# Performance work log

Measured on AMD Instinct MI355X. Metric: run time of the kernel, lower is better.

## Reference

```python
import jax, jax.numpy as jnp
import numpy as np

H = 12
D_MODEL = 768
D_K = D_MODEL // H  # 64


def setup_inputs() -> dict:
    key = jax.random.key(0)
    ks = jax.random.split(key, 16)
    B, S, D = 4, 1024, D_MODEL
    scale = 1.0 / np.sqrt(D)
    inp = {
        "query": jax.random.normal(ks[0], (B, S, D), jnp.float32),
        "key": jax.random.normal(ks[1], (B, S, D), jnp.float32),
        "value": jax.random.normal(ks[2], (B, S, D), jnp.float32),
        "times": jax.random.normal(ks[3], (2, B, S, D), jnp.float32),
        # learned params (Linear weights stored torch-style [out, in])
        "Wq": jax.random.normal(ks[4], (D, D), jnp.float32) * scale,
        "bq": jnp.zeros((D,), jnp.float32),
        "Wk": jax.random.normal(ks[5], (D, D), jnp.float32) * scale,
        "bk": jnp.zeros((D,), jnp.float32),
        "Wv": jax.random.normal(ks[6], (D, D), jnp.float32) * scale,
        "bv": jnp.zeros((D,), jnp.float32),
        "Wt": jax.random.normal(ks[7], (D, D), jnp.float32) * scale,
        "bt": jnp.zeros((D,), jnp.float32),
        "Wo": jax.random.normal(ks[8], (D, D), jnp.float32) * scale,
        "bo": jnp.zeros((D,), jnp.float32),
    }
    return inp


def _split_heads(x, B, S):
    # [B,S,D] -> [B,H,S,D_K]
    return x.reshape(B, S, H, D_K).transpose(0, 2, 1, 3)


def reference(query, key, value, times, Wq, bq, Wk, bk, Wv, bv, Wt, bt, Wo, bo):
    B, S, D = query.shape
    inv_sqrt_dk = 1.0 / jnp.sqrt(jnp.asarray(D_K, query.dtype))
    # q/k/v projections are identical across time-loop iterations; hoist them.
    q = _split_heads(query @ Wq.T + bq, B, S)   # [B,H,S,dk]
    k = _split_heads(key @ Wk.T + bk, B, S)
    v = _split_heads(value @ Wv.T + bv, B, S)
    x = jnp.zeros_like(q)
    n_times = times.shape[0]
    for i in range(n_times):  # small fixed loop over time embeddings
        t = _split_heads(times[i] @ Wt.T + bt, B, S)
        # dual-score attention: query.time + query.key, each scaled by 1/sqrt(d_k)
        scores = (jnp.einsum('bhqd,bhkd->bhqk', q, t)
                  + jnp.einsum('bhqd,bhkd->bhqk', q, k)) * inv_sqrt_dk
        p = jax.nn.softmax(scores, axis=-1)
        x = x + jnp.einsum('bhqk,bhkd->bhqd', p, v)
    x = x.transpose(0, 2, 1, 3).reshape(B, S, H * D_K)
    return x @ Wo.T + bo
```

## Files before the change

kernel.cpp:

```cpp
#include <hip/hip_runtime.h>
#include <hip/hip_fp16.h>

typedef _Float16 v8h __attribute__((ext_vector_type(8)));
typedef _Float16 v4h __attribute__((ext_vector_type(4)));
typedef _Float16 v2h __attribute__((ext_vector_type(2)));
typedef float v4f __attribute__((ext_vector_type(4)));

#define MFMA_F16 __builtin_amdgcn_mfma_f32_16x16x32_f16
#define EXP2F __builtin_amdgcn_exp2f

__device__ static inline v2h pkrtz(float a, float b) {
  return __builtin_bit_cast(v2h, __builtin_amdgcn_cvt_pkrtz(a, b));
}

__device__ static inline void async_copy16(const void* g, void* l) {
  __builtin_amdgcn_global_load_lds(
      (const __attribute__((address_space(1))) void*)g,
      (__attribute__((address_space(3))) void*)l, 16, 0, 0);
}

struct CastArgs {
  const float* src[10];
  _Float16* dst[10];
  int start[11];
  float scale[10];
};
__global__ void cast_all(CastArgs a) {
  const int g = blockIdx.x * 256 + threadIdx.x;
  if (g >= a.start[10]) return;
  int z = 0;
  #pragma unroll
  for (int i = 1; i < 10; ++i) if (g >= a.start[i]) z = i;
  const int i0 = g - a.start[z];
  const float sc = a.scale[z];
  const float* s = a.src[z] + (size_t)i0 * 8;
  const float4 f0 = *(const float4*)s;
  const float4 f1 = *(const float4*)(s + 4);
  v8h o = {(_Float16)(f0.x * sc), (_Float16)(f0.y * sc),
           (_Float16)(f0.z * sc), (_Float16)(f0.w * sc),
           (_Float16)(f1.x * sc), (_Float16)(f1.y * sc),
           (_Float16)(f1.z * sc), (_Float16)(f1.w * sc)};
  *(v8h*)(a.dst[z] + (size_t)i0 * 8) = o;
}

struct GemmArgs {
  const _Float16* A1[4]; const _Float16* A2[4];
  const _Float16* W1[4]; const _Float16* W2[4];
  const float* b1[4];    const float* b2[4];
  void* out[4];
  float bscale[4];
  int K[4];
  int mode[4];
};

template <int MT>
__global__ __launch_bounds__(256) void gemm_mt(GemmArgs g) {
  constexpr int iA = MT / 32;
  constexpr int NMT = MT / 32;
  __shared__ _Float16 a_lds[MT * 64];
  __shared__ _Float16 w_lds[128 * 64];
  const int z = blockIdx.z;
  const int KK = g.K[z];
  const int tid = threadIdx.x;
  const int w = tid >> 6, lane = tid & 63, quad = lane >> 4, l16 = lane & 15;
  const int m0 = blockIdx.x * MT, n0 = blockIdx.y * 128;
  const int wm = (w >> 1) * (MT / 2), wn = (w & 1) * 64;

  size_t srcOff[4]; int ldsOff[4];
  #pragma unroll
  for (int i = 0; i < 4; ++i) {
    const int c = i * 256 + tid, row = c >> 3, slot = c & 7;
    srcOff[i] = (size_t)row * 768 + (size_t)((slot ^ (row & 7)) * 8);
    ldsOff[i] = (i * 256 + w * 64) * 8;
  }

  v4f acc[NMT][4] = {};

  for (int k0 = 0; k0 < KK; k0 += 64) {
    const _Float16* Asrc = (k0 < 768) ? g.A1[z] : g.A2[z];
    const _Float16* Wsrc = (k0 < 768) ? g.W1[z] : g.W2[z];
    const int kc = (k0 < 768) ? k0 : k0 - 768;
    __syncthreads();
    #pragma unroll
    for (int i = 0; i < 4; ++i) {
      if (i < iA)
        async_copy16(Asrc + (size_t)m0 * 768 + kc + srcOff[i], &a_lds[ldsOff[i]]);
      async_copy16(Wsrc + (size_t)n0 * 768 + kc + srcOff[i], &w_lds[ldsOff[i]]);
    }
    __syncthreads();

    #pragma unroll
    for (int kh = 0; kh < 2; ++kh) {
      v8h af[NMT], bf[4];
      #pragma unroll
      for (int mt = 0; mt < NMT; ++mt) {
        const int r = wm + mt * 16 + l16;
        af[mt] = *(const v8h*)&a_lds[r * 64 + (((kh * 4 + quad) ^ (r & 7)) * 8)];
      }
      #pragma unroll
      for (int nt = 0; nt < 4; ++nt) {
        const int r = wn + nt * 16 + l16;
        bf[nt] = *(const v8h*)&w_lds[r * 64 + (((kh * 4 + quad) ^ (r & 7)) * 8)];
      }
      #pragma unroll
      for (int mt = 0; mt < NMT; ++mt)
        #pragma unroll
        for (int nt = 0; nt < 4; ++nt)
          acc[mt][nt] = MFMA_F16(af[mt], bf[nt], acc[mt][nt], 0, 0, 0);
    }
  }

  const int mode = g.mode[z];
  #pragma unroll
  for (int nt = 0; nt < 4; ++nt) {
    const int col = n0 + wn + nt * 16 + l16;
    float bv = g.b1[z][col] * g.bscale[z];
    if (g.b2[z]) bv += g.b2[z][col];
    if (mode == 1) {
      _Float16* outp = (_Float16*)g.out[z];
      const int h = col >> 6, dk = col & 63;
      #pragma unroll
      for (int mt = 0; mt < NMT; ++mt) {
        const int row = m0 + wm + mt * 16 + quad * 4;
        const int b = row >> 10, s = row & 1023;
        const int sp = (s & ~31) | ((s & 12) << 1) | ((s & 16) >> 2);
        v4h pack = {(_Float16)(acc[mt][nt][0] + bv), (_Float16)(acc[mt][nt][1] + bv),
                    (_Float16)(acc[mt][nt][2] + bv), (_Float16)(acc[mt][nt][3] + bv)};
        *(v4h*)&outp[(size_t)((b * 12 + h) * 64 + dk) * 1024 + sp] = pack;
      }
    } else {
      #pragma unroll
      for (int mt = 0; mt < NMT; ++mt)
        #pragma unroll
        for (int r = 0; r < 4; ++r) {
          const int row = m0 + wm + mt * 16 + quad * 4 + r;
          const float v = acc[mt][nt][r] + bv;
          if (mode == 2) ((float*)g.out[z])[(size_t)row * 768 + col] = v;
          else ((_Float16*)g.out[z])[(size_t)row * 768 + col] = (_Float16)v;
        }
    }
  }
}

__global__ __launch_bounds__(256) void attn(
    const _Float16* __restrict__ Q,
    const _Float16* __restrict__ KT0, const _Float16* __restrict__ KT1,
    const _Float16* __restrict__ Vt,
    _Float16* __restrict__ X)
{
  __shared__ _Float16 kt0[2][64 * 64];
  __shared__ _Float16 kt1[2][64 * 64];
  __shared__ _Float16 vt[2][64 * 64];

  const int tid = threadIdx.x;
  const int w = tid >> 6, lane = tid & 63, quad = lane >> 4, l16 = lane & 15;
  const int bh = blockIdx.y, b = bh / 12, h = bh % 12;
  const int q0 = blockIdx.x * 64;
  const size_t base = (size_t)b * 1024 * 768 + h * 64;

  const _Float16* KT0b = KT0 + base;
  const _Float16* KT1b = KT1 + base;
  const _Float16* Vtb = Vt + (size_t)bh * 64 * 1024;

  size_t ktOff[2], vOff[2]; int ldsOff[2];
  #pragma unroll
  for (int i = 0; i < 2; ++i) {
    const int c = i * 256 + w * 64 + lane, row = c >> 3, slot = c & 7;
    const int logical = slot ^ (row & 7);
    ktOff[i] = (size_t)row * 768 + (size_t)(logical * 8);
    vOff[i] = (size_t)row * 1024 + (size_t)(logical * 8);
    ldsOff[i] = c * 8;
  }
  auto stage = [&](int kv0, int buf) {
    #pragma unroll
    for (int i = 0; i < 2; ++i) {
      async_copy16(KT0b + (size_t)kv0 * 768 + ktOff[i], &kt0[buf][ldsOff[i]]);
      async_copy16(KT1b + (size_t)kv0 * 768 + ktOff[i], &kt1[buf][ldsOff[i]]);
      async_copy16(Vtb + (size_t)kv0 + vOff[i], &vt[buf][ldsOff[i]]);
    }
  };

  const _Float16* Qw = Q + base + (size_t)(q0 + w * 16) * 768;
  const v8h qf0 = *(const v8h*)(Qw + (size_t)l16 * 768 + quad * 8);
  const v8h qf1 = *(const v8h*)(Qw + (size_t)l16 * 768 + 32 + quad * 8);

  const _Float16 one = (_Float16)1.f;
  const v8h ones8 = {one, one, one, one, one, one, one, one};
  v4f o[2][4] = {};
  v4f osum[2] = {};

  auto body = [&](int cc, const _Float16* k0p, const _Float16* k1p,
                  const _Float16* vp) {
    __syncthreads();
    if (cc < 15) stage((cc + 1) * 64, (cc + 1) & 1);

    v4f s[2][4];
    #pragma unroll
    for (int kvt = 0; kvt < 4; ++kvt) {
      const int r = kvt * 16 + l16, rw = r & 7;
      const v8h k00 = *(const v8h*)&k0p[r * 64 + ((quad ^ rw) * 8)];
      const v8h k01 = *(const v8h*)&k0p[r * 64 + (((4 + quad) ^ rw) * 8)];
      const v8h k10 = *(const v8h*)&k1p[r * 64 + ((quad ^ rw) * 8)];
      const v8h k11 = *(const v8h*)&k1p[r * 64 + (((4 + quad) ^ rw) * 8)];
      s[0][kvt] = MFMA_F16(k00, qf0, v4f{}, 0, 0, 0);
      s[0][kvt] = MFMA_F16(k01, qf1, s[0][kvt], 0, 0, 0);
      s[1][kvt] = MFMA_F16(k10, qf0, v4f{}, 0, 0, 0);
      s[1][kvt] = MFMA_F16(k11, qf1, s[1][kvt], 0, 0, 0);
    }

    v8h pb8[2][2];
    #pragma unroll
    for (int t = 0; t < 2; ++t)
      #pragma unroll
      for (int gg = 0; gg < 2; ++gg) {
        const v4f sa = s[t][gg * 2], sb = s[t][gg * 2 + 1];
        const v2h a0 = pkrtz(EXP2F(sa[0]), EXP2F(sa[1]));
        const v2h a1 = pkrtz(EXP2F(sa[2]), EXP2F(sa[3]));
        const v2h b0 = pkrtz(EXP2F(sb[0]), EXP2F(sb[1]));
        const v2h b1 = pkrtz(EXP2F(sb[2]), EXP2F(sb[3]));
        pb8[t][gg] = v8h{a0[0], a0[1], a1[0], a1[1], b0[0], b0[1], b1[0], b1[1]};
        osum[t] = MFMA_F16(ones8, pb8[t][gg], osum[t], 0, 0, 0);
      }

    #pragma unroll
    for (int dkt = 0; dkt < 4; ++dkt) {
      const int row = dkt * 16 + l16, rw = row & 7;
      #pragma unroll
      for (int gg = 0; gg < 2; ++gg) {
        const int slot = (gg * 4 + quad) ^ rw;
        const v8h vv = *(const v8h*)&vp[row * 64 + slot * 8];
        o[0][dkt] = MFMA_F16(vv, pb8[0][gg], o[0][dkt], 0, 0, 0);
        o[1][dkt] = MFMA_F16(vv, pb8[1][gg], o[1][dkt], 0, 0, 0);
      }
    }
  };

  stage(0, 0);
  for (int it = 0; it < 8; ++it) {
    body(it * 2, &kt0[0][0], &kt1[0][0], &vt[0][0]);
    body(it * 2 + 1, &kt0[1][0], &kt1[1][0], &vt[1][0]);
  }

  const float i0 = 1.0f / osum[0][0], i1 = 1.0f / osum[1][0];

  _Float16* Xw = X + base + (size_t)(q0 + w * 16 + l16) * 768;
  #pragma unroll
  for (int dkt = 0; dkt < 4; ++dkt) {
    v4h pack;
    #pragma unroll
    for (int r = 0; r < 4; ++r)
      pack[r] = (_Float16)(o[0][dkt][r] * i0 + o[1][dkt][r] * i1);
    *(v4h*)&Xw[dkt * 16 + quad * 4] = pack;
  }
}

extern "C" void kernel_launch(void* const* d_in, const int* in_sizes, int n_in,
                              void* d_out, int out_size, void* d_ws, size_t ws_size,
                              hipStream_t stream) {
  const float* query = (const float*)d_in[0];
  const float* key   = (const float*)d_in[1];
  const float* value = (const float*)d_in[2];
  const float* times = (const float*)d_in[3];
  const float* Wq = (const float*)d_in[4];  const float* bq = (const float*)d_in[5];
  const float* Wk = (const float*)d_in[6];  const float* bk = (const float*)d_in[7];
  const float* Wv = (const float*)d_in[8];  const float* bv = (const float*)d_in[9];
  const float* Wt = (const float*)d_in[10]; const float* bt = (const float*)d_in[11];
  const float* Wo = (const float*)d_in[12]; const float* bo = (const float*)d_in[13];
  float* out = (float*)d_out;

  const size_t NELEM = (size_t)4096 * 768;
  const size_t WELEM = (size_t)768 * 768;
  const float QSCALE = 0.125f * 1.4426950408889634f;

  char* ws = (char*)d_ws;
  size_t off = 0;
  auto alloc = [&](size_t bytes) {
    void* p = ws + off; off += (bytes + 255) & ~(size_t)255; return p;
  };
  _Float16* qh  = (_Float16*)alloc(NELEM * 2);
  _Float16* kh  = (_Float16*)alloc(NELEM * 2);
  _Float16* vh  = (_Float16*)alloc(NELEM * 2);
  _Float16* wqh = (_Float16*)alloc(WELEM * 2);
  _Float16* wkh = (_Float16*)alloc(WELEM * 2);
  _Float16* wvh = (_Float16*)alloc(WELEM * 2);
  _Float16* wth = (_Float16*)alloc(WELEM * 2);
  _Float16* woh = (_Float16*)alloc(WELEM * 2);
  _Float16* Qh  = (_Float16*)alloc(NELEM * 2);
  _Float16* KT0 = (_Float16*)alloc(NELEM * 2);
  _Float16* KT1 = (_Float16*)alloc(NELEM * 2);
  _Float16* Vt  = (_Float16*)alloc(NELEM * 2);
  _Float16* t0h = (_Float16*)d_out;
  _Float16* t1h = t0h + NELEM;
  _Float16* Xh = qh;

  CastArgs ca = {};
  const int nA8 = (int)(NELEM / 8), nW8 = (int)(WELEM / 8);
  const float* csrc[10] = {query, key, value, times, times + NELEM, Wq, Wk, Wv, Wt, Wo};
  _Float16* cdst[10] = {qh, kh, vh, t0h, t1h, wqh, wkh, wvh, wth, woh};
  int acc8 = 0;
  for (int i = 0; i < 10; ++i) {
    ca.src[i] = csrc[i]; ca.dst[i] = cdst[i];
    ca.start[i] = acc8;
    acc8 += (i < 5) ? nA8 : nW8;
    ca.scale[i] = (i == 5) ? QSCALE : 1.0f;
  }
  ca.start[10] = acc8;
  cast_all<<<dim3((acc8 + 255) / 256), 256, 0, stream>>>(ca);

  GemmArgs pa = {};
  pa.A1[0] = t0h; pa.A2[0] = kh; pa.W1[0] = wth; pa.W2[0] = wkh;
  pa.b1[0] = bt; pa.b2[0] = bk; pa.out[0] = KT0; pa.bscale[0] = 1.0f;
  pa.K[0] = 1536; pa.mode[0] = 0;
  pa.A1[1] = t1h; pa.A2[1] = kh; pa.W1[1] = wth; pa.W2[1] = wkh;
  pa.b1[1] = bt; pa.b2[1] = bk; pa.out[1] = KT1; pa.bscale[1] = 1.0f;
  pa.K[1] = 1536; pa.mode[1] = 0;
  pa.A1[2] = qh; pa.A2[2] = qh; pa.W1[2] = wqh; pa.W2[2] = wqh;
  pa.b1[2] = bq; pa.b2[2] = nullptr; pa.out[2] = Qh; pa.bscale[2] = QSCALE;
  pa.K[2] = 768; pa.mode[2] = 0;
  pa.A1[3] = vh; pa.A2[3] = vh; pa.W1[3] = wvh; pa.W2[3] = wvh;
  pa.b1[3] = bv; pa.b2[3] = nullptr; pa.out[3] = Vt; pa.bscale[3] = 1.0f;
  pa.K[3] = 768; pa.mode[3] = 1;
  gemm_mt<128><<<dim3(32, 6, 4), 256, 0, stream>>>(pa);

  attn<<<dim3(16, 48), 256, 0, stream>>>(Qh, KT0, KT1, Vt, Xh);

  GemmArgs oa = {};
  oa.A1[0] = Xh; oa.A2[0] = Xh; oa.W1[0] = woh; oa.W2[0] = woh;
  oa.b1[0] = bo; oa.b2[0] = nullptr; oa.out[0] = out; oa.bscale[0] = 1.0f;
  oa.K[0] = 768; oa.mode[0] = 2;
  gemm_mt<64><<<dim3(64, 6, 1), 256, 0, stream>>>(oa);
}
```

Baseline: 231.7 us.

## Remap attention workgroup order, precompute LDS addresses, add MFMA priority hints

Merges the three LDS buffers into one array and precomputes the swizzled byte offsets once, so the inner loop uses constant-offset addressing. The staging pointers are advanced incrementally instead of recomputing offsets each step. The workgroup index is remapped so neighbouring workgroups are spread across heads and batches, which may change cache locality across the chip. s_setprio is raised around the MFMA sections to favour matrix issue. These are scheduling and address-overhead tweaks that change no arithmetic, but the remap could hurt L2 reuse of K and V.

Result: no change. 228.6 us (-1.3%).

```diff
diff --git a/kernel.cpp b/kernel.cpp
--- a/kernel.cpp
+++ b/kernel.cpp
@@ -148,19 +148,20 @@
     const _Float16* __restrict__ Vt,
     _Float16* __restrict__ X)
 {
-  __shared__ _Float16 kt0[2][64 * 64];
-  __shared__ _Float16 kt1[2][64 * 64];
-  __shared__ _Float16 vt[2][64 * 64];
+  __shared__ _Float16 lds[6 * 4096];
 
   const int tid = threadIdx.x;
   const int w = tid >> 6, lane = tid & 63, quad = lane >> 4, l16 = lane & 15;
-  const int bh = blockIdx.y, b = bh / 12, h = bh % 12;
-  const int q0 = blockIdx.x * 64;
+
+  const int orig = blockIdx.y * 16 + blockIdx.x;
+  const int wgid = (orig & 7) * 96 + (orig >> 3);
+  const int bh = wgid >> 4, q0 = (wgid & 15) * 64;
+  const int b = bh / 12, h = bh % 12;
   const size_t base = (size_t)b * 1024 * 768 + h * 64;
 
-  const _Float16* KT0b = KT0 + base;
-  const _Float16* KT1b = KT1 + base;
-  const _Float16* Vtb = Vt + (size_t)bh * 64 * 1024;
+  const _Float16* k0s = KT0 + base;
+  const _Float16* k1s = KT1 + base;
+  const _Float16* vs  = Vt + (size_t)bh * 64 * 1024;
 
   size_t ktOff[2], vOff[2]; int ldsOff[2];
   #pragma unroll
@@ -171,42 +172,53 @@
     vOff[i] = (size_t)row * 1024 + (size_t)(logical * 8);
     ldsOff[i] = c * 8;
   }
-  auto stage = [&](int kv0, int buf) {
+  auto stage = [&](int buf) {
     #pragma unroll
     for (int i = 0; i < 2; ++i) {
-      async_copy16(KT0b + (size_t)kv0 * 768 + ktOff[i], &kt0[buf][ldsOff[i]]);
-      async_copy16(KT1b + (size_t)kv0 * 768 + ktOff[i], &kt1[buf][ldsOff[i]]);
-      async_copy16(Vtb + (size_t)kv0 + vOff[i], &vt[buf][ldsOff[i]]);
-    }
+      async_copy16(k0s + ktOff[i], &lds[buf * 4096 + ldsOff[i]]);
+      async_copy16(k1s + ktOff[i], &lds[8192 + buf * 4096 + ldsOff[i]]);
+      async_copy16(vs + vOff[i], &lds[16384 + buf * 4096 + ldsOff[i]]);
+    }
+    k0s += 64 * 768; k1s += 64 * 768; vs += 64;
   };
 
   const _Float16* Qw = Q + base + (size_t)(q0 + w * 16) * 768;
   const v8h qf0 = *(const v8h*)(Qw + (size_t)l16 * 768 + quad * 8);
   const v8h qf1 = *(const v8h*)(Qw + (size_t)l16 * 768 + 32 + quad * 8);
+
+  int ra0[4], ra1[4];
+  #pragma unroll
+  for (int t = 0; t < 4; ++t) {
+    const int r = t * 16 + l16, rw = r & 7;
+    ra0[t] = (r * 64 + ((quad ^ rw) * 8)) * 2;
+    ra1[t] = ra0[t] ^ 64;
+  }
 
   const _Float16 one = (_Float16)1.f;
   const v8h ones8 = {one, one, one, one, one, one, one, one};
   v4f o[2][4] = {};
   v4f osum[2] = {};
 
-  auto body = [&](int cc, const _Float16* k0p, const _Float16* k1p,
-                  const _Float16* vp) {
+  auto body = [&](int B, bool doStage) {
     __syncthreads();
-    if (cc < 15) stage((cc + 1) * 64, (cc + 1) & 1);
+    if (doStage) stage((B == 0) ? 1 : 0);
+
+    const char* L = (const char*)lds;
 
     v4f s[2][4];
+    __builtin_amdgcn_s_setprio(1);
     #pragma unroll
     for (int kvt = 0; kvt < 4; ++kvt) {
-      const int r = kvt * 16 + l16, rw = r & 7;
-      const v8h k00 = *(const v8h*)&k0p[r * 64 + ((quad ^ rw) * 8)];
-      const v8h k01 = *(const v8h*)&k0p[r * 64 + (((4 + quad) ^ rw) * 8)];
-      const v8h k10 = *(const v8h*)&k1p[r * 64 + ((quad ^ rw) * 8)];
-      const v8h k11 = *(const v8h*)&k1p[r * 64 + (((4 + quad) ^ rw) * 8)];
+      const v8h k00 = *(const v8h*)(L + B + ra0[kvt]);
+      const v8h k01 = *(const v8h*)(L + B + ra1[kvt]);
+      const v8h k10 = *(const v8h*)(L + 16384 + B + ra0[kvt]);
+      const v8h k11 = *(const v8h*)(L + 16384 + B + ra1[kvt]);
       s[0][kvt] = MFMA_F16(k00, qf0, v4f{}, 0, 0, 0);
       s[0][kvt] = MFMA_F16(k01, qf1, s[0][kvt], 0, 0, 0);
       s[1][kvt] = MFMA_F16(k10, qf0, v4f{}, 0, 0, 0);
       s[1][kvt] = MFMA_F16(k11, qf1, s[1][kvt], 0, 0, 0);
     }
+    __builtin_amdgcn_s_setprio(0);
 
     v8h pb8[2][2];
     #pragma unroll
@@ -222,24 +234,26 @@
         osum[t] = MFMA_F16(ones8, pb8[t][gg], osum[t], 0, 0, 0);
       }
 
+    __builtin_amdgcn_s_setprio(1);
     #pragma unroll
     for (int dkt = 0; dkt < 4; ++dkt) {
-      const int row = dkt * 16 + l16, rw = row & 7;
-      #pragma unroll
-      for (int gg = 0; gg < 2; ++gg) {
-        const int slot = (gg * 4 + quad) ^ rw;
-        const v8h vv = *(const v8h*)&vp[row * 64 + slot * 8];
-        o[0][dkt] = MFMA_F16(vv, pb8[0][gg], o[0][dkt], 0, 0, 0);
-        o[1][dkt] = MFMA_F16(vv, pb8[1][gg], o[1][dkt], 0, 0, 0);
-      }
-    }
+      const v8h v0 = *(const v8h*)(L + 32768 + B + ra0[dkt]);
+      const v8h v1 = *(const v8h*)(L + 32768 + B + ra1[dkt]);
+      o[0][dkt] = MFMA_F16(v0, pb8[0][0], o[0][dkt], 0, 0, 0);
+      o[0][dkt] = MFMA_F16(v1, pb8[0][1], o[0][dkt], 0, 0, 0);
+      o[1][dkt] = MFMA_F16(v0, pb8[1][0], o[1][dkt], 0, 0, 0);
+      o[1][dkt] = MFMA_F16(v1, pb8[1][1], o[1][dkt], 0, 0, 0);
+    }
+    __builtin_amdgcn_s_setprio(0);
   };
 
-  stage(0, 0);
-  for (int it = 0; it < 8; ++it) {
-    body(it * 2, &kt0[0][0], &kt1[0][0], &vt[0][0]);
-    body(it * 2 + 1, &kt0[1][0], &kt1[1][0], &vt[1][0]);
-  }
+  stage(0);
+  for (int it = 0; it < 7; ++it) {
+    body(0, true);
+    body(8192, true);
+  }
+  body(0, true);
+  body(8192, false);
 
   const float i0 = 1.0f / osum[0][0], i1 = 1.0f / osum[1][0];
 
```
